# Kernel tuning notes

Hardware: AMD Instinct MI355X
Metric: run time of the kernel (lower is better)

## Reference

```python
import jax, jax.numpy as jnp
import numpy as np

N_ITEMS = 262144
INPUT_DIM = 128
N_CODEBOOKS = 3
CODEBOOK_SIZE = 256


def setup_inputs() -> dict:
    key = jax.random.key(0)
    kx, kc = jax.random.split(key)
    x = jax.random.normal(kx, (N_ITEMS, INPUT_DIM), dtype=jnp.float32)
    # xavier_uniform for (codebook_size, input_dim) weights
    limit = float(np.sqrt(6.0 / (CODEBOOK_SIZE + INPUT_DIM)))
    codebooks = jax.random.uniform(
        kc, (N_CODEBOOKS, CODEBOOK_SIZE, INPUT_DIM),
        minval=-limit, maxval=limit, dtype=jnp.float32)
    return {"x": x, "codebooks": codebooks}


def reference(x, codebooks):
    """Residual VQ: sequentially quantize residual against each codebook.

    x: (n_items, d) float; codebooks: (n_cb, K, d) float.
    Returns (indices (n_items, n_cb) int32, quantized (n_items, d)).
    """
    residual = x
    quantized = jnp.zeros_like(x)
    idx_list = []
    for i in range(codebooks.shape[0]):  # small fixed loop over codebooks
        cb = codebooks[i]  # (K, d)
        # squared L2 distance; argmin equals argmin of torch.cdist (p=2)
        d2 = (jnp.sum(residual * residual, axis=-1, keepdims=True)
              - 2.0 * (residual @ cb.T)
              + jnp.sum(cb * cb, axis=-1))  # (n_items, K)
        idx = jnp.argmin(d2, axis=1)  # (n_items,)
        q = cb[idx]                   # gather: (n_items, d)
        quantized = quantized + q
        residual = residual - q
        idx_list.append(idx)
    return jnp.stack(idx_list, axis=1), quantized
```

## Files before the change

kernel.cpp:

```cpp
#include <hip/hip_runtime.h>
#include <math.h>


constexpr int kItems = 262144;
constexpr int kDim   = 128;
constexpr int kNcb   = 3;
constexpr int kK     = 256;
constexpr int kBlock = 256;
constexpr int kBatch = 16;
constexpr int NPH    = 32;

typedef float sf4 __attribute__((ext_vector_type(4)));

__device__ __forceinline__ float sq_rn(float x) {
    return __builtin_fmaf(x, x, 0.0f);
}

template <typename F>
__device__ __forceinline__ float np_pairwise128(F term) {
    float r0 = term(0), r1 = term(1), r2 = term(2), r3 = term(3),
          r4 = term(4), r5 = term(5), r6 = term(6), r7 = term(7);
    #pragma unroll
    for (int i = 8; i < 128; i += 8) {
        r0 = r0 + term(i + 0); r1 = r1 + term(i + 1);
        r2 = r2 + term(i + 2); r3 = r3 + term(i + 3);
        r4 = r4 + term(i + 4); r5 = r5 + term(i + 5);
        r6 = r6 + term(i + 6); r7 = r7 + term(i + 7);
    }
    return ((r0 + r1) + (r2 + r3)) + ((r4 + r5) + (r6 + r7));
}

__global__ void rvq_prep(const float* __restrict__ cb,
                         float* __restrict__ Bt,
                         float* __restrict__ cbT2)
{
    const int tid = blockIdx.x * 256 + threadIdx.x;
    const int d = tid & 3;
    const int l = (tid >> 2) & 63;
    const int v = (tid >> 8) & 3;
    const int p = (tid >> 10) & 31;
    const int c = tid >> 15;
    cbT2[tid] = cb[((size_t)c * kK + 64 * v + l) * kDim + (4 * p + d)];
    if (tid < kNcb * kK) {
        const float* row = cb + (size_t)tid * kDim;
        Bt[tid] = np_pairwise128([&](int jj) { return sq_rn(row[jj]); });
    }
}

#define X16(X) X(0) X(1) X(2) X(3) X(4) X(5) X(6) X(7) \
  X(8) X(9) X(10) X(11) X(12) X(13) X(14) X(15)

#define MDECL(i) float m##i##_0 = 0.f, m##i##_1 = 0.f, \
                       m##i##_2 = 0.f, m##i##_3 = 0.f;

#define FMAS(i, RV) \
    m##i##_0 = __builtin_fmaf(RV.x, q0.x, m##i##_0); \
    m##i##_0 = __builtin_fmaf(RV.y, q0.y, m##i##_0); \
    m##i##_0 = __builtin_fmaf(RV.z, q0.z, m##i##_0); \
    m##i##_0 = __builtin_fmaf(RV.w, q0.w, m##i##_0); \
    m##i##_1 = __builtin_fmaf(RV.x, q1.x, m##i##_1); \
    m##i##_1 = __builtin_fmaf(RV.y, q1.y, m##i##_1); \
    m##i##_1 = __builtin_fmaf(RV.z, q1.z, m##i##_1); \
    m##i##_1 = __builtin_fmaf(RV.w, q1.w, m##i##_1); \
    m##i##_2 = __builtin_fmaf(RV.x, q2.x, m##i##_2); \
    m##i##_2 = __builtin_fmaf(RV.y, q2.y, m##i##_2); \
    m##i##_2 = __builtin_fmaf(RV.z, q2.z, m##i##_2); \
    m##i##_2 = __builtin_fmaf(RV.w, q2.w, m##i##_2); \
    m##i##_3 = __builtin_fmaf(RV.x, q3.x, m##i##_3); \
    m##i##_3 = __builtin_fmaf(RV.y, q3.y, m##i##_3); \
    m##i##_3 = __builtin_fmaf(RV.z, q3.z, m##i##_3); \
    m##i##_3 = __builtin_fmaf(RV.w, q3.w, m##i##_3);

#define RVDECL(i) sf4 rv##i;
#define DOFMA(i)  FMAS(i, rv##i)

#define ARGMIN(i) { \
    const float Ai = __shfl(Areg, (i)); \
    float bv = __builtin_fmaf(-2.0f, m##i##_0, Ai) + B0; \
    int   bx = lane; \
    float dd = __builtin_fmaf(-2.0f, m##i##_1, Ai) + B1; \
    if (dd < bv) { bv = dd; bx = 64 + lane; } \
    dd = __builtin_fmaf(-2.0f, m##i##_2, Ai) + B2; \
    if (dd < bv) { bv = dd; bx = 128 + lane; } \
    dd = __builtin_fmaf(-2.0f, m##i##_3, Ai) + B3; \
    if (dd < bv) { bv = dd; bx = 192 + lane; } \
    _Pragma("unroll") \
    for (int off = 32; off; off >>= 1) { \
        const float ov = __shfl_xor(bv, off); \
        const int   ox = __shfl_xor(bx, off); \
        const bool take = (ov < bv) || (ov == bv && ox < bx); \
        bv = take ? ov : bv; bx = take ? ox : bx; \
    } \
    if (c == 0)      sel0 = (lane == (i)) ? bx : sel0; \
    else if (c == 1) sel1 = (lane == (i)) ? bx : sel1; \
    else             sel2 = (lane == (i)) ? bx : sel2; }

__global__ __launch_bounds__(kBlock, 2) void rvq_kernel(
    const float* __restrict__ x,
    const float* __restrict__ cb,
    const float* __restrict__ Bt,
    const float* __restrict__ cbT2,
    float* __restrict__ out)
{
    const int t = threadIdx.x;
    const int lane = t & 63;
    const int wid = blockIdx.x * (kBlock / 64) + (t >> 6);
    const size_t ibase = (size_t)wid * kBatch;

    float* out_idx = out;
    float* out_q   = out + (size_t)kItems * kNcb;

    const float* xb = x + ibase * kDim;
    float*       qb = out_q + ibase * kDim;

    int sel0 = 0, sel1 = 0, sel2 = 0;

    #pragma unroll 1
    for (int c = 0; c < kNcb; ++c) {
        const float* rb_ = (c == 0) ? xb : (const float*)qb;
        const float* cbTc = cbT2 + (size_t)c * 32768;

        const uint64_t rbu = (uint64_t)(const void*)rb_;
        const uint32_t blo = __builtin_amdgcn_readfirstlane((uint32_t)rbu);
        const uint32_t bhi = __builtin_amdgcn_readfirstlane((uint32_t)(rbu >> 32));
        const uint64_t sbase = ((uint64_t)bhi << 32) | (uint64_t)blo;

        float Areg = 0.0f;
        if (lane < kBatch) {
            const float4* rr = (const float4*)(rb_ + (size_t)lane * kDim);
            float4 ra = rr[0], rb2v = rr[1];
            float a0 = sq_rn(ra.x),   a1 = sq_rn(ra.y),
                  a2 = sq_rn(ra.z),   a3 = sq_rn(ra.w),
                  a4 = sq_rn(rb2v.x), a5 = sq_rn(rb2v.y),
                  a6 = sq_rn(rb2v.z), a7 = sq_rn(rb2v.w);
            #pragma unroll
            for (int g = 1; g < 16; ++g) {
                ra = rr[2 * g]; rb2v = rr[2 * g + 1];
                a0 = a0 + sq_rn(ra.x);   a1 = a1 + sq_rn(ra.y);
                a2 = a2 + sq_rn(ra.z);   a3 = a3 + sq_rn(ra.w);
                a4 = a4 + sq_rn(rb2v.x); a5 = a5 + sq_rn(rb2v.y);
                a6 = a6 + sq_rn(rb2v.z); a7 = a7 + sq_rn(rb2v.w);
            }
            Areg = ((a0 + a1) + (a2 + a3)) + ((a4 + a5) + (a6 + a7));
        }

        X16(MDECL)
        #pragma unroll 1
        for (int p = 0; p < NPH; ++p) {
            const float4* cbq = (const float4*)(cbTc + ((size_t)p * 4) * 256)
                                + lane;
            const float4 q0 = cbq[0];
            const float4 q1 = cbq[64];
            const float4 q2 = cbq[128];
            const float4 q3 = cbq[192];

            const uint64_t sb = sbase + (uint64_t)(16 * p);
            X16(RVDECL)
            asm volatile(
                "s_load_dwordx4 %[r0],  %[b], 0x0\n\t"
                "s_load_dwordx4 %[r1],  %[b], 0x200\n\t"
                "s_load_dwordx4 %[r2],  %[b], 0x400\n\t"
                "s_load_dwordx4 %[r3],  %[b], 0x600\n\t"
                "s_load_dwordx4 %[r4],  %[b], 0x800\n\t"
                "s_load_dwordx4 %[r5],  %[b], 0xa00\n\t"
                "s_load_dwordx4 %[r6],  %[b], 0xc00\n\t"
                "s_load_dwordx4 %[r7],  %[b], 0xe00\n\t"
                "s_load_dwordx4 %[r8],  %[b], 0x1000\n\t"
                "s_load_dwordx4 %[r9],  %[b], 0x1200\n\t"
                "s_load_dwordx4 %[r10], %[b], 0x1400\n\t"
                "s_load_dwordx4 %[r11], %[b], 0x1600\n\t"
                "s_load_dwordx4 %[r12], %[b], 0x1800\n\t"
                "s_load_dwordx4 %[r13], %[b], 0x1a00\n\t"
                "s_load_dwordx4 %[r14], %[b], 0x1c00\n\t"
                "s_load_dwordx4 %[r15], %[b], 0x1e00\n\t"
                "s_waitcnt lgkmcnt(0)"
                : [r0]"=s"(rv0),  [r1]"=s"(rv1),  [r2]"=s"(rv2),
                  [r3]"=s"(rv3),  [r4]"=s"(rv4),  [r5]"=s"(rv5),
                  [r6]"=s"(rv6),  [r7]"=s"(rv7),  [r8]"=s"(rv8),
                  [r9]"=s"(rv9),  [r10]"=s"(rv10), [r11]"=s"(rv11),
                  [r12]"=s"(rv12), [r13]"=s"(rv13), [r14]"=s"(rv14),
                  [r15]"=s"(rv15)
                : [b]"s"(sb)
                : "memory");

            X16(DOFMA)
        }

        const float* Btc = Bt + c * kK;
        const float B0 = Btc[lane],       B1 = Btc[64 + lane];
        const float B2 = Btc[128 + lane], B3 = Btc[192 + lane];
        X16(ARGMIN)

        if (c < 2) {
            #pragma unroll 1
            for (int i = 0; i < kBatch; ++i) {
                const int s = __shfl((c == 0) ? sel0 : sel1, i);
                const float* cwrow = cb + ((size_t)c * kK + s) * kDim;
                const float2 w = *(const float2*)(cwrow + 2 * lane);
                float* dr = qb + (size_t)i * kDim;
                const float* sr = (c == 0) ? (xb + (size_t)i * kDim)
                                           : (const float*)dr;
                float2 rv = *(const float2*)(sr + 2 * lane);
                rv.x = rv.x - w.x;
                rv.y = rv.y - w.y;
                *(float2*)(dr + 2 * lane) = rv;
            }
            asm volatile("s_waitcnt vmcnt(0)" ::: "memory");
            __builtin_amdgcn_s_dcache_inv();
        }
    }

    #pragma unroll 1
    for (int i = 0; i < kBatch; ++i) {
        const int s0 = __shfl(sel0, i);
        const int s1 = __shfl(sel1, i);
        const int s2 = __shfl(sel2, i);
        const float2 u = *(const float2*)(cb + ((size_t)0 * kK + s0) * kDim + 2 * lane);
        const float2 v = *(const float2*)(cb + ((size_t)1 * kK + s1) * kDim + 2 * lane);
        const float2 w = *(const float2*)(cb + ((size_t)2 * kK + s2) * kDim + 2 * lane);
        float2 o;
        o.x = (u.x + v.x) + w.x;
        o.y = (u.y + v.y) + w.y;
        *(float2*)(qb + (size_t)i * kDim + 2 * lane) = o;
        if (lane == 0) {
            out_idx[(ibase + i) * kNcb + 0] = (float)s0;
            out_idx[(ibase + i) * kNcb + 1] = (float)s1;
            out_idx[(ibase + i) * kNcb + 2] = (float)s2;
        }
    }
}

extern "C" void kernel_launch(void* const* d_in, const int* in_sizes, int n_in,
                              void* d_out, int out_size, void* d_ws, size_t ws_size,
                              hipStream_t stream) {
    const float* x  = (const float*)d_in[0];
    const float* cb = (const float*)d_in[1];
    float* out = (float*)d_out;
    float* Bt  = (float*)d_ws;
    float* cbT2 = (float*)d_ws + 1024;
    rvq_prep<<<384, 256, 0, stream>>>(cb, Bt, cbT2);
    rvq_kernel<<<kItems / (kBatch * 4), kBlock, 0, stream>>>(x, cb, Bt, cbT2, out);
}
```

Measured before the change: 702.4 us.

## Software-pipeline scalar residual loads and codebook loads across phases

Splits the per-phase scalar loads of residual rows into two halves and issues each half before the FMAs of the other half, so scalar memory latency overlaps with compute. Codebook vector loads are double-buffered (qa_/qb_) one phase ahead, and the loop is unrolled by two with a peeled epilogue. This raises SGPR and VGPR pressure and depends on the hand-ordered s_waitcnt placement being correct.

```diff
diff --git a/kernel.cpp b/kernel.cpp
--- a/kernel.cpp
+++ b/kernel.cpp
@@ -53,26 +53,85 @@
 #define MDECL(i) float m##i##_0 = 0.f, m##i##_1 = 0.f, \
                        m##i##_2 = 0.f, m##i##_3 = 0.f;
 
-#define FMAS(i, RV) \
-    m##i##_0 = __builtin_fmaf(RV.x, q0.x, m##i##_0); \
-    m##i##_0 = __builtin_fmaf(RV.y, q0.y, m##i##_0); \
-    m##i##_0 = __builtin_fmaf(RV.z, q0.z, m##i##_0); \
-    m##i##_0 = __builtin_fmaf(RV.w, q0.w, m##i##_0); \
-    m##i##_1 = __builtin_fmaf(RV.x, q1.x, m##i##_1); \
-    m##i##_1 = __builtin_fmaf(RV.y, q1.y, m##i##_1); \
-    m##i##_1 = __builtin_fmaf(RV.z, q1.z, m##i##_1); \
-    m##i##_1 = __builtin_fmaf(RV.w, q1.w, m##i##_1); \
-    m##i##_2 = __builtin_fmaf(RV.x, q2.x, m##i##_2); \
-    m##i##_2 = __builtin_fmaf(RV.y, q2.y, m##i##_2); \
-    m##i##_2 = __builtin_fmaf(RV.z, q2.z, m##i##_2); \
-    m##i##_2 = __builtin_fmaf(RV.w, q2.w, m##i##_2); \
-    m##i##_3 = __builtin_fmaf(RV.x, q3.x, m##i##_3); \
-    m##i##_3 = __builtin_fmaf(RV.y, q3.y, m##i##_3); \
-    m##i##_3 = __builtin_fmaf(RV.z, q3.z, m##i##_3); \
-    m##i##_3 = __builtin_fmaf(RV.w, q3.w, m##i##_3);
-
-#define RVDECL(i) sf4 rv##i;
-#define DOFMA(i)  FMAS(i, rv##i)
+#define FMAS(i, RV, Q) \
+    m##i##_0 = __builtin_fmaf(RV.x, (Q##0).x, m##i##_0); \
+    m##i##_0 = __builtin_fmaf(RV.y, (Q##0).y, m##i##_0); \
+    m##i##_0 = __builtin_fmaf(RV.z, (Q##0).z, m##i##_0); \
+    m##i##_0 = __builtin_fmaf(RV.w, (Q##0).w, m##i##_0); \
+    m##i##_1 = __builtin_fmaf(RV.x, (Q##1).x, m##i##_1); \
+    m##i##_1 = __builtin_fmaf(RV.y, (Q##1).y, m##i##_1); \
+    m##i##_1 = __builtin_fmaf(RV.z, (Q##1).z, m##i##_1); \
+    m##i##_1 = __builtin_fmaf(RV.w, (Q##1).w, m##i##_1); \
+    m##i##_2 = __builtin_fmaf(RV.x, (Q##2).x, m##i##_2); \
+    m##i##_2 = __builtin_fmaf(RV.y, (Q##2).y, m##i##_2); \
+    m##i##_2 = __builtin_fmaf(RV.z, (Q##2).z, m##i##_2); \
+    m##i##_2 = __builtin_fmaf(RV.w, (Q##2).w, m##i##_2); \
+    m##i##_3 = __builtin_fmaf(RV.x, (Q##3).x, m##i##_3); \
+    m##i##_3 = __builtin_fmaf(RV.y, (Q##3).y, m##i##_3); \
+    m##i##_3 = __builtin_fmaf(RV.z, (Q##3).z, m##i##_3); \
+    m##i##_3 = __builtin_fmaf(RV.w, (Q##3).w, m##i##_3);
+
+#define FHALF_LO(Q) FMAS(0,rv0,Q) FMAS(1,rv1,Q) FMAS(2,rv2,Q) FMAS(3,rv3,Q) \
+                    FMAS(4,rv4,Q) FMAS(5,rv5,Q) FMAS(6,rv6,Q) FMAS(7,rv7,Q)
+#define FHALF_HI(Q) FMAS(8,rv8,Q) FMAS(9,rv9,Q) FMAS(10,rv10,Q) FMAS(11,rv11,Q) \
+                    FMAS(12,rv12,Q) FMAS(13,rv13,Q) FMAS(14,rv14,Q) FMAS(15,rv15,Q)
+
+#define QDECL(P) float4 P##0, P##1, P##2, P##3;
+#define QLOAD(P, PH) { \
+    const float4* cbq_ = (const float4*)(cbTc + ((size_t)(PH) * 4) * 256) + lane; \
+    P##0 = cbq_[0]; P##1 = cbq_[64]; P##2 = cbq_[128]; P##3 = cbq_[192]; }
+
+#define SLOAD_PRO(BASE) asm volatile( \
+    "s_waitcnt lgkmcnt(0)\n\t" \
+    "s_load_dwordx4 %[r0], %[b], 0x0\n\t" \
+    "s_load_dwordx4 %[r1], %[b], 0x200\n\t" \
+    "s_load_dwordx4 %[r2], %[b], 0x400\n\t" \
+    "s_load_dwordx4 %[r3], %[b], 0x600\n\t" \
+    "s_load_dwordx4 %[r4], %[b], 0x800\n\t" \
+    "s_load_dwordx4 %[r5], %[b], 0xa00\n\t" \
+    "s_load_dwordx4 %[r6], %[b], 0xc00\n\t" \
+    "s_load_dwordx4 %[r7], %[b], 0xe00" \
+    : [r0]"=&s"(rv0), [r1]"=&s"(rv1), [r2]"=&s"(rv2), [r3]"=&s"(rv3), \
+      [r4]"=&s"(rv4), [r5]"=&s"(rv5), [r6]"=&s"(rv6), [r7]"=&s"(rv7) \
+    : [b]"s"(BASE) : "memory")
+
+#define SLOAD_HI(BASE) asm volatile( \
+    "s_waitcnt lgkmcnt(0)\n\t" \
+    "s_load_dwordx4 %[r8],  %[b], 0x1000\n\t" \
+    "s_load_dwordx4 %[r9],  %[b], 0x1200\n\t" \
+    "s_load_dwordx4 %[r10], %[b], 0x1400\n\t" \
+    "s_load_dwordx4 %[r11], %[b], 0x1600\n\t" \
+    "s_load_dwordx4 %[r12], %[b], 0x1800\n\t" \
+    "s_load_dwordx4 %[r13], %[b], 0x1a00\n\t" \
+    "s_load_dwordx4 %[r14], %[b], 0x1c00\n\t" \
+    "s_load_dwordx4 %[r15], %[b], 0x1e00" \
+    : [r8]"=&s"(rv8),  [r9]"=&s"(rv9),  [r10]"=&s"(rv10), [r11]"=&s"(rv11), \
+      [r12]"=&s"(rv12), [r13]"=&s"(rv13), [r14]"=&s"(rv14), [r15]"=&s"(rv15), \
+      [t0]"+s"(rv0), [t1]"+s"(rv1), [t2]"+s"(rv2), [t3]"+s"(rv3), \
+      [t4]"+s"(rv4), [t5]"+s"(rv5), [t6]"+s"(rv6), [t7]"+s"(rv7) \
+    : [b]"s"(BASE) : "memory")
+
+#define SLOAD_LO(BASE) asm volatile( \
+    "s_waitcnt lgkmcnt(0)\n\t" \
+    "s_load_dwordx4 %[r0], %[b], 0x0\n\t" \
+    "s_load_dwordx4 %[r1], %[b], 0x200\n\t" \
+    "s_load_dwordx4 %[r2], %[b], 0x400\n\t" \
+    "s_load_dwordx4 %[r3], %[b], 0x600\n\t" \
+    "s_load_dwordx4 %[r4], %[b], 0x800\n\t" \
+    "s_load_dwordx4 %[r5], %[b], 0xa00\n\t" \
+    "s_load_dwordx4 %[r6], %[b], 0xc00\n\t" \
+    "s_load_dwordx4 %[r7], %[b], 0xe00" \
+    : [r0]"=&s"(rv0), [r1]"=&s"(rv1), [r2]"=&s"(rv2), [r3]"=&s"(rv3), \
+      [r4]"=&s"(rv4), [r5]"=&s"(rv5), [r6]"=&s"(rv6), [r7]"=&s"(rv7), \
+      [t8]"+s"(rv8),  [t9]"+s"(rv9),  [t10]"+s"(rv10), [t11]"+s"(rv11), \
+      [t12]"+s"(rv12), [t13]"+s"(rv13), [t14]"+s"(rv14), [t15]"+s"(rv15) \
+    : [b]"s"(BASE) : "memory")
+
+#define SWAIT_HI() asm volatile( \
+    "s_waitcnt lgkmcnt(0)" \
+    : [t8]"+s"(rv8),  [t9]"+s"(rv9),  [t10]"+s"(rv10), [t11]"+s"(rv11), \
+      [t12]"+s"(rv12), [t13]"+s"(rv13), [t14]"+s"(rv14), [t15]"+s"(rv15) \
+    :: "memory")
 
 #define ARGMIN(i) { \
     const float Ai = __shfl(Areg, (i)); \
@@ -125,6 +184,13 @@
         const uint32_t bhi = __builtin_amdgcn_readfirstlane((uint32_t)(rbu >> 32));
         const uint64_t sbase = ((uint64_t)bhi << 32) | (uint64_t)blo;
 
+        sf4 rv0, rv1, rv2, rv3, rv4, rv5, rv6, rv7,
+            rv8, rv9, rv10, rv11, rv12, rv13, rv14, rv15;
+
+        SLOAD_PRO(sbase);
+        QDECL(qa_) QDECL(qb_)
+        QLOAD(qa_, 0)
+
         float Areg = 0.0f;
         if (lane < kBatch) {
             const float4* rr = (const float4*)(rb_ + (size_t)lane * kDim);
@@ -146,45 +212,33 @@
 
         X16(MDECL)
         #pragma unroll 1
-        for (int p = 0; p < NPH; ++p) {
-            const float4* cbq = (const float4*)(cbTc + ((size_t)p * 4) * 256)
-                                + lane;
-            const float4 q0 = cbq[0];
-            const float4 q1 = cbq[64];
-            const float4 q2 = cbq[128];
-            const float4 q3 = cbq[192];
-
-            const uint64_t sb = sbase + (uint64_t)(16 * p);
-            X16(RVDECL)
-            asm volatile(
-                "s_load_dwordx4 %[r0],  %[b], 0x0\n\t"
-                "s_load_dwordx4 %[r1],  %[b], 0x200\n\t"
-                "s_load_dwordx4 %[r2],  %[b], 0x400\n\t"
-                "s_load_dwordx4 %[r3],  %[b], 0x600\n\t"
-                "s_load_dwordx4 %[r4],  %[b], 0x800\n\t"
-                "s_load_dwordx4 %[r5],  %[b], 0xa00\n\t"
-                "s_load_dwordx4 %[r6],  %[b], 0xc00\n\t"
-                "s_load_dwordx4 %[r7],  %[b], 0xe00\n\t"
-                "s_load_dwordx4 %[r8],  %[b], 0x1000\n\t"
-                "s_load_dwordx4 %[r9],  %[b], 0x1200\n\t"
-                "s_load_dwordx4 %[r10], %[b], 0x1400\n\t"
-                "s_load_dwordx4 %[r11], %[b], 0x1600\n\t"
-                "s_load_dwordx4 %[r12], %[b], 0x1800\n\t"
-                "s_load_dwordx4 %[r13], %[b], 0x1a00\n\t"
-                "s_load_dwordx4 %[r14], %[b], 0x1c00\n\t"
-                "s_load_dwordx4 %[r15], %[b], 0x1e00\n\t"
-                "s_waitcnt lgkmcnt(0)"
-                : [r0]"=s"(rv0),  [r1]"=s"(rv1),  [r2]"=s"(rv2),
-                  [r3]"=s"(rv3),  [r4]"=s"(rv4),  [r5]"=s"(rv5),
-                  [r6]"=s"(rv6),  [r7]"=s"(rv7),  [r8]"=s"(rv8),
-                  [r9]"=s"(rv9),  [r10]"=s"(rv10), [r11]"=s"(rv11),
-                  [r12]"=s"(rv12), [r13]"=s"(rv13), [r14]"=s"(rv14),
-                  [r15]"=s"(rv15)
-                : [b]"s"(sb)
-                : "memory");
-
-            X16(DOFMA)
-        }
+        for (int pp = 0; pp < NPH / 2 - 1; ++pp) {
+            const int pe = 2 * pp;
+            const int po = 2 * pp + 1;
+            const int pn = pe + 2;
+
+            SLOAD_HI(sbase + (uint64_t)(16 * pe));
+            QLOAD(qb_, po)
+            FHALF_LO(qa_)
+            SLOAD_LO(sbase + (uint64_t)(16 * po));
+            FHALF_HI(qa_)
+
+            SLOAD_HI(sbase + (uint64_t)(16 * po));
+            QLOAD(qa_, pn)
+            FHALF_LO(qb_)
+            SLOAD_LO(sbase + (uint64_t)(16 * pn));
+            FHALF_HI(qb_)
+        }
+
+        SLOAD_HI(sbase + (uint64_t)(16 * 30));
+        QLOAD(qb_, 31)
+        FHALF_LO(qa_)
+        SLOAD_LO(sbase + (uint64_t)(16 * 31));
+        FHALF_HI(qa_)
+        SLOAD_HI(sbase + (uint64_t)(16 * 31));
+        FHALF_LO(qb_)
+        SWAIT_HI();
+        FHALF_HI(qb_)
 
         const float* Btc = Bt + c * kK;
         const float B0 = Btc[lane],       B1 = Btc[64 + lane];
```

Result: no change. 705.9 us (+0.5%).
